# Kernel tuning notes

Measured on AMD Instinct MI355X. Metric: run time of the kernel, lower is better.

Reference implementation:

```python
import jax, jax.numpy as jnp
import numpy as np

B, N, C = 4, 4096, 16
HID, HEADS, OUT = 64, 4, 64
NEG = -1e16

def setup_inputs() -> dict:
    key = jax.random.key(0)
    ks = jax.random.split(key, 7)
    x = jax.random.normal(ks[0], (B, N, C), dtype=jnp.float32)
    # sparse-ish binary adjacency with self-loops, stored dense as in the torch module
    graph = (jax.random.randint(ks[1], (N, N), 0, 2)).astype(jnp.float32)
    graph = jnp.maximum(graph, jnp.eye(N, dtype=jnp.float32))
    # per-head Linear weights (bias=False) and the per-layer bias parameter b
    Ws = jax.random.normal(ks[2], (HEADS, C, HID), dtype=jnp.float32)   # W.weight.T per head
    bs = jax.random.normal(ks[3], (HEADS, HID), dtype=jnp.float32)
    W_out = jax.random.normal(ks[4], (HEADS * HID, OUT), dtype=jnp.float32)
    b_out = jax.random.normal(ks[5], (OUT,), dtype=jnp.float32)
    return {"x": x, "graph": graph, "Ws": Ws, "bs": bs, "W_out": W_out, "b_out": b_out}

def _gat_layer(x, graph, W, b):
    # x: [B,N,Cin], W: [Cin,D], b: [D]
    h = jnp.einsum('bnc,cd->bnd', x, W)                      # [B,N,D]
    s = jnp.einsum('bnd,bmd->bnm', h, h) * graph[None]       # [B,N,N]
    s = jnp.where(s == 0.0, NEG, s)                          # masked_fill(eq 0, -1e16)
    attn = jax.nn.softmax(s, axis=2)
    return jnp.einsum('bnm,bmd->bnd', attn, h) + b

def _leaky_relu(x):
    return jnp.where(x >= 0, x, 0.2 * x)

def reference(x, graph, Ws, bs, W_out, b_out):
    # multi-head layers, concatenated on feature dim (head-major)
    heads = jax.vmap(lambda W, b: _gat_layer(x, graph, W, b))(Ws, bs)  # [H,B,N,D]
    cat = jnp.transpose(heads, (1, 2, 0, 3)).reshape(B, N, HEADS * HID)
    cat = _leaky_relu(cat)
    out = _gat_layer(cat, graph, W_out, b_out)
    return _leaky_relu(out)
```

## Files before the change

### kernel.cpp

```cpp
#include <hip/hip_runtime.h>

typedef unsigned short u16;
typedef unsigned int u32;
typedef unsigned long long u64;
typedef __attribute__((ext_vector_type(8))) short bf16x8;
typedef __attribute__((ext_vector_type(4))) float f32x4;
typedef __attribute__((ext_vector_type(16))) float f32x16;

#define NEGF  -1.0e38f
#define MINIT -1.0e30f
#define LOG2E 1.4426950408889634f

__device__ __forceinline__ u16 f2bf(float x) {
  union { float f; u32 u; } v; v.f = x;
  u32 r = v.u + 0x7fffu + ((v.u >> 16) & 1u);
  return (u16)(r >> 16);
}
__device__ __forceinline__ float bf2f(u16 b) {
  union { u32 u; float f; } v; v.u = ((u32)b) << 16;
  return v.f;
}
__device__ __forceinline__ float bcast(u32 u) {
  union { u32 u; float f; } v; v.u = u; return v.f;
}
__device__ __forceinline__ u32 cvtpk(float a, float b) {
  u32 r;
  asm("v_cvt_pk_bf16_f32 %0, %1, %2" : "=v"(r) : "v"(a), "v"(b));
  return r;
}
__device__ __forceinline__ float vexp2(float x) {
  float r;
  asm("v_exp_f32 %0, %1" : "=v"(r) : "v"(x));
  return r;
}
__device__ __forceinline__ float fmax3(float a, float b, float c) {
  return fmaxf(fmaxf(a, b), c);
}
__device__ __forceinline__ float leaky(float x) { return x >= 0.f ? x : 0.2f * x; }

__device__ __forceinline__ void gload16(const void* g, void* l) {
  __builtin_amdgcn_global_load_lds(
      (const __attribute__((address_space(1))) u32*)(unsigned long long)g,
      (__attribute__((address_space(3))) u32*)(u32)(unsigned long long)l,
      16, 0, 0);
}

#define GRP   1040
#define TILE  8320
#define KA_OFF 0
#define KB_OFF 8320
#define KC_OFF 16640
#define V_OFF  24960
#define SMEM_BYTES 58240

__global__ __launch_bounds__(256) void pack_kernel(const float* __restrict__ graph,
                                                   u64* __restrict__ bits) {
  const int n = blockIdx.x;
  const int w = threadIdx.x >> 6, lane = threadIdx.x & 63;
  const float* gr = graph + (size_t)n * 4096;
  for (int j = 0; j < 16; ++j) {
    const int wd = j * 4 + w;
    u64 m = __ballot(gr[wd * 64 + lane] != 0.0f);
    if (lane == 0) bits[(size_t)wd * 4096 + n] = m;
  }
}

__global__ __launch_bounds__(256) void h1_kernel(const float* __restrict__ x,
                                                 const float* __restrict__ Ws,
                                                 u16* __restrict__ h1a, u16* __restrict__ h1b,
                                                 u16* __restrict__ h1c) {
  const int blk = blockIdx.x;
  const int h = threadIdx.x >> 6, d = threadIdx.x & 63;
  const float* xr = x + (size_t)blk * 16;
  const float* Wp = Ws + h * (16 * 64) + d;
  float acc = 0.f;
  #pragma unroll
  for (int c = 0; c < 16; ++c) acc += xr[c] * Wp[c * 64];
  const int b = blk >> 12, n = blk & 4095;
  const size_t o = ((size_t)(b * 4 + h) * 4096 + n) * 64 + d;
  u16 a = f2bf(acc);
  float r1 = acc - bf2f(a);
  u16 bq = f2bf(r1);
  float r2 = r1 - bf2f(bq);
  h1a[o] = a; h1b[o] = bq; h1c[o] = f2bf(r2);
}

__global__ __launch_bounds__(256) void transpose_kernel(const u16* __restrict__ src,
                                                        u16* __restrict__ dst) {
  const int p = blockIdx.y, n0 = blockIdx.x * 64;
  const u16* s = src + (size_t)p * 4096 * 64;
  u16* d = dst + (size_t)p * 4096 * 64;
  __shared__ u16 tile[64][66];
  const int col = threadIdx.x & 63, r4 = threadIdx.x >> 6;
  #pragma unroll
  for (int i = 0; i < 16; ++i) {
    const int r = i * 4 + r4;
    tile[r][col] = s[(size_t)(n0 + r) * 64 + col];
  }
  __syncthreads();
  const int cs = (col & 51) | ((col & 4) << 1) | ((col & 8) >> 1);
  #pragma unroll
  for (int i = 0; i < 16; ++i) {
    const int r = i * 4 + r4;
    d[(size_t)r * 4096 + n0 + cs] = tile[col][r];
  }
}

__global__ __launch_bounds__(256) void h2_kernel(const float* __restrict__ cat,
                                                 const float* __restrict__ Wout,
                                                 u16* __restrict__ h2a, u16* __restrict__ h2b,
                                                 u16* __restrict__ h2c) {
  const int row = blockIdx.x * 4 + (threadIdx.x >> 6);
  const int d = threadIdx.x & 63;
  const float* cr = cat + (size_t)row * 256;
  float acc = 0.f;
  for (int c4 = 0; c4 < 64; ++c4) {
    const float4 cv = *(const float4*)(cr + c4 * 4);
    acc += cv.x * Wout[(c4 * 4 + 0) * 64 + d];
    acc += cv.y * Wout[(c4 * 4 + 1) * 64 + d];
    acc += cv.z * Wout[(c4 * 4 + 2) * 64 + d];
    acc += cv.w * Wout[(c4 * 4 + 3) * 64 + d];
  }
  const size_t o = (size_t)row * 64 + d;
  u16 a = f2bf(acc);
  float r1 = acc - bf2f(a);
  u16 bq = f2bf(r1);
  float r2 = r1 - bf2f(bq);
  h2a[o] = a; h2b[o] = bq; h2c[o] = f2bf(r2);
}

template <int LAYER>
__global__ __launch_bounds__(256) void attn_kernel(
    const u16* __restrict__ Ha, const u16* __restrict__ Hb, const u16* __restrict__ Hc,
    const u16* __restrict__ HaT, const u16* __restrict__ HbT,
    const u64* __restrict__ bits, const float* __restrict__ bias,
    float* __restrict__ outp, float* __restrict__ pm, float* __restrict__ pl) {
  constexpr int NCH = (LAYER == 1) ? 64 : 16;
  const int orig = blockIdx.x + 32 * blockIdx.y;
  const int sid = (orig & 7) * 64 + (orig >> 3);
  const int bx = sid & 31;
  const int py = sid >> 5;
  const int pass = (LAYER == 1) ? py : (py & 3);
  const int chg0 = (LAYER == 1) ? 0 : ((py >> 2) * 16);

  const int t = threadIdx.x;
  const int wq = t >> 6;
  const int lane = t & 63;
  const int c = lane & 31;
  const int g1 = lane >> 5;
  const int qbase = bx * 128 + wq * 32;
  const int q = qbase + c;
  const size_t poffb = (size_t)pass * (4096 * 64) * 2;

  __shared__ f32x4 smem_v[SMEM_BYTES / 16];
  char* smem = (char*)smem_v;

  const int srow = lane >> 3;
  const int scol = ((lane & 7) ^ srow) << 4;
  const char* gKa = (const char*)Ha + poffb;
  const char* gKb = (const char*)Hb + poffb;
  const char* gKc = (const char*)Hc + poffb;
  const char* gVa = (const char*)HaT + poffb;
  const char* gVb = (const char*)HbT + poffb;

  auto stageK = [&](int chg) {
    const size_t cb = (size_t)chg * 8192;
    #pragma unroll
    for (int ii = 0; ii < 2; ++ii) {
      const int g = wq * 2 + ii;
      const size_t so = cb + (size_t)(g * 8 + srow) * 128 + scol;
      const int dofs = g * GRP;
      gload16(gKa + so, smem + KA_OFF + dofs);
      gload16(gKb + so, smem + KB_OFF + dofs);
      gload16(gKc + so, smem + KC_OFF + dofs);
    }
  };
  auto stageV = [&](int chg, int buf) {
    const char* gsrc = (wq >> 1) ? gVb : gVa;
    char* dbase = smem + V_OFF + buf * 16640 + (wq >> 1) * TILE;
    const size_t cb = (size_t)chg * 128;
    #pragma unroll
    for (int ii = 0; ii < 4; ++ii) {
      const int g = (wq & 1) * 4 + ii;
      const size_t so = cb + (size_t)(g * 8 + srow) * 8192 + scol;
      gload16(gsrc + so, dbase + g * GRP);
    }
  };

  bf16x8 qf[3][4];
  {
    const char* qra = (const char*)Ha + poffb + (size_t)q * 128 + 16 * g1;
    const char* qrb = (const char*)Hb + poffb + (size_t)q * 128 + 16 * g1;
    const char* qrc = (const char*)Hc + poffb + (size_t)q * 128 + 16 * g1;
    #pragma unroll
    for (int kk = 0; kk < 4; ++kk) {
      qf[0][kk] = *(const bf16x8*)(qra + kk * 32);
      qf[1][kk] = *(const bf16x8*)(qrb + kk * 32);
      qf[2][kk] = *(const bf16x8*)(qrc + kk * 32);
    }
  }

  const u64* bqp = bits + q;

  const int swz = (c & 7) << 4;
  int iK[4];
  #pragma unroll
  for (int kk = 0; kk < 4; ++kk)
    iK[kk] = c * 128 + ((c >> 3) << 4) + ((32 * kk + 16 * g1) ^ swz);

  const f32x16 z16 = {};
  f32x16 Of0, Of1;
  #pragma unroll
  for (int r = 0; r < 16; ++r) { Of0[r] = 0.f; Of1[r] = 0.f; }
  float mrow = MINIT, lrow = 0.f;

  stageK(chg0);
  stageV(chg0, 0);
  u64 mcur = bqp[(size_t)chg0 * 4096];
  asm volatile("s_waitcnt vmcnt(0)" ::: "memory");
  __syncthreads();

  #pragma unroll 1
  for (int ch = 0; ch < NCH; ++ch) {
    const int chg = chg0 + ch;
    __builtin_amdgcn_sched_barrier(0);
    f32x16 s0, s1;
    __builtin_amdgcn_s_setprio(1);
    #pragma unroll
    for (int kk = 0; kk < 4; ++kk) {
      const char* kp0 = smem + iK[kk];
      const char* kp1 = smem + 4 * GRP + iK[kk];
      const bf16x8 ka0 = *(const bf16x8*)(kp0 + KA_OFF);
      const bf16x8 kb0 = *(const bf16x8*)(kp0 + KB_OFF);
      const bf16x8 kc0 = *(const bf16x8*)(kp0 + KC_OFF);
      const bf16x8 ka1 = *(const bf16x8*)(kp1 + KA_OFF);
      const bf16x8 kb1 = *(const bf16x8*)(kp1 + KB_OFF);
      const bf16x8 kc1 = *(const bf16x8*)(kp1 + KC_OFF);
      s0 = __builtin_amdgcn_mfma_f32_32x32x16_bf16(ka0, qf[2][kk], kk ? s0 : z16, 0, 0, 0);
      s1 = __builtin_amdgcn_mfma_f32_32x32x16_bf16(ka1, qf[2][kk], kk ? s1 : z16, 0, 0, 0);
      s0 = __builtin_amdgcn_mfma_f32_32x32x16_bf16(kb0, qf[1][kk], s0, 0, 0, 0);
      s1 = __builtin_amdgcn_mfma_f32_32x32x16_bf16(kb1, qf[1][kk], s1, 0, 0, 0);
      s0 = __builtin_amdgcn_mfma_f32_32x32x16_bf16(kc0, qf[0][kk], s0, 0, 0, 0);
      s1 = __builtin_amdgcn_mfma_f32_32x32x16_bf16(kc1, qf[0][kk], s1, 0, 0, 0);
      s0 = __builtin_amdgcn_mfma_f32_32x32x16_bf16(ka0, qf[1][kk], s0, 0, 0, 0);
      s1 = __builtin_amdgcn_mfma_f32_32x32x16_bf16(ka1, qf[1][kk], s1, 0, 0, 0);
      s0 = __builtin_amdgcn_mfma_f32_32x32x16_bf16(kb0, qf[0][kk], s0, 0, 0, 0);
      s1 = __builtin_amdgcn_mfma_f32_32x32x16_bf16(kb1, qf[0][kk], s1, 0, 0, 0);
      s0 = __builtin_amdgcn_mfma_f32_32x32x16_bf16(ka0, qf[0][kk], s0, 0, 0, 0);
      s1 = __builtin_amdgcn_mfma_f32_32x32x16_bf16(ka1, qf[0][kk], s1, 0, 0, 0);
    }
    __builtin_amdgcn_s_setprio(0);
    __builtin_amdgcn_sched_barrier(0);
    __builtin_amdgcn_s_barrier();
    __builtin_amdgcn_sched_barrier(0);
    if (ch + 1 < NCH) {
      stageK(chg + 1);
      stageV(chg + 1, (ch + 1) & 1);
    }
    __builtin_amdgcn_sched_barrier(0);

    const u32 a0 = (u32)(mcur >> (4 * g1));
    const u32 a1 = (u32)(mcur >> (32 + 4 * g1));
    #pragma unroll
    for (int r = 0; r < 16; ++r) {
      const int off = (r & 3) + 8 * (r >> 2);
      s0[r] = ((a0 >> off) & 1u) ? s0[r] : NEGF;
      s1[r] = ((a1 >> off) & 1u) ? s1[r] : NEGF;
    }
    float t0 = fmax3(s0[0], s0[1], s0[2]);
    float t1 = fmax3(s0[3], s0[4], s0[5]);
    float t2 = fmax3(s0[6], s0[7], s0[8]);
    float t3 = fmax3(s0[9], s0[10], s0[11]);
    float t4 = fmax3(s0[12], s0[13], s0[14]);
    float t5 = fmax3(s0[15], s1[0], s1[1]);
    float t6 = fmax3(s1[2], s1[3], s1[4]);
    float t7 = fmax3(s1[5], s1[6], s1[7]);
    float t8 = fmax3(s1[8], s1[9], s1[10]);
    float t9 = fmax3(s1[11], s1[12], s1[13]);
    float ta = fmaxf(s1[14], s1[15]);
    float u0 = fmax3(t0, t1, t2);
    float u1 = fmax3(t3, t4, t5);
    float u2 = fmax3(t6, t7, t8);
    float u3 = fmax3(t9, ta, u0);
    float mm = fmax3(u1, u2, u3);
    mm = fmaxf(mm, __shfl_xor(mm, 32));
    if (!__all(mm <= mrow + 8.f)) {
      const float mn = fmaxf(mrow, mm);
      const float scl = vexp2((mrow - mn) * LOG2E);
      #pragma unroll
      for (int r = 0; r < 16; ++r) { Of0[r] *= scl; Of1[r] *= scl; }
      lrow *= scl;
      mrow = mn;
    }
    if (LAYER == 1) {
      const float mL = mrow * LOG2E;
      #pragma unroll
      for (int r = 0; r < 16; ++r) {
        s0[r] = vexp2(__builtin_fmaf(s0[r], LOG2E, -mL));
        s1[r] = vexp2(__builtin_fmaf(s1[r], LOG2E, -mL));
      }
    } else {
      #pragma unroll
      for (int r = 0; r < 16; ++r) {
        s0[r] = vexp2((s0[r] - mrow) * LOG2E);
        s1[r] = vexp2((s1[r] - mrow) * LOG2E);
      }
    }
    {
      float r4[4];
      #pragma unroll
      for (int j = 0; j < 4; ++j)
        r4[j] = ((s0[4*j] + s0[4*j+1]) + (s0[4*j+2] + s0[4*j+3]))
              + ((s1[4*j] + s1[4*j+1]) + (s1[4*j+2] + s1[4*j+3]));
      float rs = (r4[0] + r4[1]) + (r4[2] + r4[3]);
      rs += __shfl_xor(rs, 32);
      lrow += rs;
    }

    bf16x8 pa[4], pb[4];
    #pragma unroll
    for (int kk = 0; kk < 4; ++kk) {
      const f32x16& sm = (kk >> 1) ? s1 : s0;
      const int rb = 8 * (kk & 1);
      union { u32 w[4]; bf16x8 v; } ua, ub;
      #pragma unroll
      for (int j = 0; j < 4; ++j) {
        const float p0 = sm[rb + 2*j], p1 = sm[rb + 2*j + 1];
        const u32 h = cvtpk(p0, p1);
        ua.w[j] = h;
        const float h0f = bcast(h << 16);
        const float h1f = bcast(h & 0xffff0000u);
        ub.w[j] = cvtpk(p0 - h0f, p1 - h1f);
      }
      pa[kk] = ua.v; pb[kk] = ub.v;
    }

    const char* vbase = smem + V_OFF + (ch & 1) * 16640;
    __builtin_amdgcn_s_setprio(1);
    #pragma unroll
    for (int kk = 0; kk < 4; ++kk) {
      const char* vp0 = vbase + iK[kk];
      const char* vp1 = vbase + 4 * GRP + iK[kk];
      const bf16x8 va0 = *(const bf16x8*)(vp0);
      const bf16x8 vb0 = *(const bf16x8*)(vp0 + TILE);
      const bf16x8 va1 = *(const bf16x8*)(vp1);
      const bf16x8 vb1 = *(const bf16x8*)(vp1 + TILE);
      Of0 = __builtin_amdgcn_mfma_f32_32x32x16_bf16(vb0, pa[kk], Of0, 0, 0, 0);
      Of1 = __builtin_amdgcn_mfma_f32_32x32x16_bf16(vb1, pa[kk], Of1, 0, 0, 0);
      Of0 = __builtin_amdgcn_mfma_f32_32x32x16_bf16(va0, pb[kk], Of0, 0, 0, 0);
      Of1 = __builtin_amdgcn_mfma_f32_32x32x16_bf16(va1, pb[kk], Of1, 0, 0, 0);
      Of0 = __builtin_amdgcn_mfma_f32_32x32x16_bf16(va0, pa[kk], Of0, 0, 0, 0);
      Of1 = __builtin_amdgcn_mfma_f32_32x32x16_bf16(va1, pa[kk], Of1, 0, 0, 0);
    }
    __builtin_amdgcn_s_setprio(0);

    u64 mnxt = 0;
    if (ch + 1 < NCH) mnxt = bqp[(size_t)(chg + 1) * 4096];
    __builtin_amdgcn_sched_barrier(0);
    if (ch + 1 < NCH) {
      asm volatile("s_waitcnt vmcnt(1)" ::: "memory");
    } else {
      asm volatile("s_waitcnt vmcnt(0)" ::: "memory");
    }
    __builtin_amdgcn_sched_barrier(0);
    __builtin_amdgcn_s_barrier();
    mcur = mnxt;
  }

  char* reg = smem + wq * 8704;
  const float inv = (LAYER == 1) ? (1.0f / lrow) : 1.0f;
  #pragma unroll
  for (int dt = 0; dt < 2; ++dt) {
    const f32x16& o = dt ? Of1 : Of0;
    #pragma unroll
    for (int i = 0; i < 4; ++i) {
      f32x4 v;
      v[0] = o[4*i+0] * inv; v[1] = o[4*i+1] * inv;
      v[2] = o[4*i+2] * inv; v[3] = o[4*i+3] * inv;
      *(f32x4*)(reg + c * 272 + (32 * dt + 8 * i + 4 * g1) * 4) = v;
    }
  }
  if (LAYER == 2 && lane < 32) {
    pm[(size_t)py * 4096 + q] = mrow;
    pl[(size_t)py * 4096 + q] = lrow;
  }
  __syncthreads();
  const int d0 = (lane & 15) * 4;
  const float* bp = (LAYER == 1) ? (bias + (pass & 3) * 64) : bias;
  #pragma unroll
  for (int qq = 0; qq < 8; ++qq) {
    const int ql = qq * 4 + (lane >> 4);
    f32x4 v = *(const f32x4*)(reg + ql * 272 + (lane & 15) * 16);
    const int qg = qbase + ql;
    if (LAYER == 1) {
      v[0] = leaky(v[0] + bp[d0 + 0]);
      v[1] = leaky(v[1] + bp[d0 + 1]);
      v[2] = leaky(v[2] + bp[d0 + 2]);
      v[3] = leaky(v[3] + bp[d0 + 3]);
      *(f32x4*)&outp[((size_t)((pass >> 2) * 4096 + qg)) * 256 + (pass & 3) * 64 + d0] = v;
    } else {
      *(f32x4*)&outp[((size_t)py * 4096 + qg) * 64 + d0] = v;
    }
  }
}

__global__ __launch_bounds__(256) void merge_kernel(
    const float* __restrict__ pO, const float* __restrict__ pm, const float* __restrict__ pl,
    const float* __restrict__ bo, float* __restrict__ dout) {
  const int t = threadIdx.x;
  const int d = t & 63;
  const int q = blockIdx.x * 4 + (t >> 6);
  const int pass = blockIdx.y;
  float m[4], l[4], o[4];
  #pragma unroll
  for (int s = 0; s < 4; ++s) {
    const size_t idx = (size_t)(s * 4 + pass) * 4096 + q;
    m[s] = pm[idx]; l[s] = pl[idx];
    o[s] = pO[idx * 64 + d];
  }
  const float M = fmaxf(fmaxf(m[0], m[1]), fmaxf(m[2], m[3]));
  float num = 0.f, den = 0.f;
  #pragma unroll
  for (int s = 0; s < 4; ++s) {
    const float w = exp2f((m[s] - M) * LOG2E);
    num += w * o[s]; den += w * l[s];
  }
  const float r = num / den + bo[d];
  dout[((size_t)pass * 4096 + q) * 64 + d] = leaky(r);
}

extern "C" void kernel_launch(void* const* d_in, const int* in_sizes, int n_in,
                              void* d_out, int out_size, void* d_ws, size_t ws_size,
                              hipStream_t stream) {
  const float* x     = (const float*)d_in[0];
  const float* graph = (const float*)d_in[1];
  const float* Ws    = (const float*)d_in[2];
  const float* bs    = (const float*)d_in[3];
  const float* W_out = (const float*)d_in[4];
  const float* b_out = (const float*)d_in[5];
  char* ws = (char*)d_ws;
  const size_t MiB = 1048576;

  u64* bits   = (u64*)(ws + 0 * MiB);
  u16* h1a    = (u16*)(ws + 2 * MiB);
  u16* h1b    = (u16*)(ws + 10 * MiB);
  u16* h1c    = (u16*)(ws + 18 * MiB);
  u16* h1aT   = (u16*)(ws + 26 * MiB);
  u16* h1bT   = (u16*)(ws + 34 * MiB);
  float* catb = (float*)(ws + 42 * MiB);
  u16* h2a    = (u16*)(ws + 58 * MiB);
  u16* h2b    = (u16*)(ws + 60 * MiB);
  u16* h2c    = (u16*)(ws + 62 * MiB);
  u16* h2aT   = (u16*)(ws + 64 * MiB);
  u16* h2bT   = (u16*)(ws + 66 * MiB);
  float* pO   = (float*)(ws + 2 * MiB);
  float* pmb  = (float*)(ws + 18 * MiB);
  float* plb  = (float*)(ws + 18 * MiB + 262144);

  pack_kernel<<<4096, 256, 0, stream>>>(graph, bits);
  h1_kernel<<<16384, 256, 0, stream>>>(x, Ws, h1a, h1b, h1c);
  transpose_kernel<<<dim3(64, 16), 256, 0, stream>>>(h1a, h1aT);
  transpose_kernel<<<dim3(64, 16), 256, 0, stream>>>(h1b, h1bT);
  attn_kernel<1><<<dim3(32, 16), 256, 0, stream>>>(h1a, h1b, h1c, h1aT, h1bT,
                                                   bits, bs, catb, nullptr, nullptr);
  h2_kernel<<<4096, 256, 0, stream>>>(catb, W_out, h2a, h2b, h2c);
  transpose_kernel<<<dim3(64, 4), 256, 0, stream>>>(h2a, h2aT);
  transpose_kernel<<<dim3(64, 4), 256, 0, stream>>>(h2b, h2bT);
  attn_kernel<2><<<dim3(32, 16), 256, 0, stream>>>(h2a, h2b, h2c, h2aT, h2bT,
                                                   bits, b_out, pO, pmb, plb);
  merge_kernel<<<dim3(1024, 4), 256, 0, stream>>>(pO, pmb, plb, b_out, (float*)d_out);
}
```

Before: 445.0 us.

## Fuse h1 projection with transposes and split softmax into two half-chunks

The h1 projection kernel now processes 64-row tiles per block, stages x in shared memory, keeps weights in registers, and writes the transposed bf16 hi/lo copies directly, replacing two separate transpose launches. In the attention loop, the mask/max/exp/sum/convert and PV MFMA work is split into two halves (s0 then s1), so MFMAs for the first half can overlap the exp work of the second. The split adds an extra max reduction and a possible extra rescale per chunk.

After: 465.5 us. 4.6% more time.

```diff
diff --git a/kernel.cpp b/kernel.cpp
--- a/kernel.cpp
+++ b/kernel.cpp
@@ -68,21 +68,49 @@
 __global__ __launch_bounds__(256) void h1_kernel(const float* __restrict__ x,
                                                  const float* __restrict__ Ws,
                                                  u16* __restrict__ h1a, u16* __restrict__ h1b,
-                                                 u16* __restrict__ h1c) {
-  const int blk = blockIdx.x;
-  const int h = threadIdx.x >> 6, d = threadIdx.x & 63;
-  const float* xr = x + (size_t)blk * 16;
-  const float* Wp = Ws + h * (16 * 64) + d;
-  float acc = 0.f;
-  #pragma unroll
-  for (int c = 0; c < 16; ++c) acc += xr[c] * Wp[c * 64];
-  const int b = blk >> 12, n = blk & 4095;
-  const size_t o = ((size_t)(b * 4 + h) * 4096 + n) * 64 + d;
-  u16 a = f2bf(acc);
-  float r1 = acc - bf2f(a);
-  u16 bq = f2bf(r1);
-  float r2 = r1 - bf2f(bq);
-  h1a[o] = a; h1b[o] = bq; h1c[o] = f2bf(r2);
+                                                 u16* __restrict__ h1c,
+                                                 u16* __restrict__ h1aT, u16* __restrict__ h1bT) {
+  const int n0 = blockIdx.x * 64;
+  const int p  = blockIdx.y;
+  const int b = p >> 2, h = p & 3;
+  const int t = threadIdx.x;
+  const int d = t & 63, rg = t >> 6;
+  __shared__ float xt[64][17];
+  __shared__ u16 ta[64][66];
+  __shared__ u16 tb[64][66];
+  {
+    const float4 v = *(const float4*)(x + ((size_t)b * 4096 + n0 + (t >> 2)) * 16 + (t & 3) * 4);
+    xt[t >> 2][(t & 3) * 4 + 0] = v.x;
+    xt[t >> 2][(t & 3) * 4 + 1] = v.y;
+    xt[t >> 2][(t & 3) * 4 + 2] = v.z;
+    xt[t >> 2][(t & 3) * 4 + 3] = v.w;
+  }
+  float Wd[16];
+  #pragma unroll
+  for (int c = 0; c < 16; ++c) Wd[c] = Ws[h * (16 * 64) + c * 64 + d];
+  __syncthreads();
+  #pragma unroll
+  for (int it = 0; it < 16; ++it) {
+    const int r = it * 4 + rg;
+    float acc = 0.f;
+    #pragma unroll
+    for (int c = 0; c < 16; ++c) acc += xt[r][c] * Wd[c];
+    const size_t o = ((size_t)p * 4096 + n0 + r) * 64 + d;
+    u16 a = f2bf(acc);
+    float r1 = acc - bf2f(a);
+    u16 bq = f2bf(r1);
+    float r2 = r1 - bf2f(bq);
+    h1a[o] = a; h1b[o] = bq; h1c[o] = f2bf(r2);
+    ta[r][d] = a; tb[r][d] = bq;
+  }
+  __syncthreads();
+  const int cs = (d & 51) | ((d & 4) << 1) | ((d & 8) >> 1);
+  #pragma unroll
+  for (int i = 0; i < 16; ++i) {
+    const int dr = i * 4 + rg;
+    h1aT[((size_t)p * 64 + dr) * 4096 + n0 + cs] = ta[d][dr];
+    h1bT[((size_t)p * 64 + dr) * 4096 + n0 + cs] = tb[d][dr];
+  }
 }
 
 __global__ __launch_bounds__(256) void transpose_kernel(const u16* __restrict__ src,
@@ -261,98 +289,81 @@
 
     const u32 a0 = (u32)(mcur >> (4 * g1));
     const u32 a1 = (u32)(mcur >> (32 + 4 * g1));
-    #pragma unroll
-    for (int r = 0; r < 16; ++r) {
-      const int off = (r & 3) + 8 * (r >> 2);
-      s0[r] = ((a0 >> off) & 1u) ? s0[r] : NEGF;
-      s1[r] = ((a1 >> off) & 1u) ? s1[r] : NEGF;
-    }
-    float t0 = fmax3(s0[0], s0[1], s0[2]);
-    float t1 = fmax3(s0[3], s0[4], s0[5]);
-    float t2 = fmax3(s0[6], s0[7], s0[8]);
-    float t3 = fmax3(s0[9], s0[10], s0[11]);
-    float t4 = fmax3(s0[12], s0[13], s0[14]);
-    float t5 = fmax3(s0[15], s1[0], s1[1]);
-    float t6 = fmax3(s1[2], s1[3], s1[4]);
-    float t7 = fmax3(s1[5], s1[6], s1[7]);
-    float t8 = fmax3(s1[8], s1[9], s1[10]);
-    float t9 = fmax3(s1[11], s1[12], s1[13]);
-    float ta = fmaxf(s1[14], s1[15]);
-    float u0 = fmax3(t0, t1, t2);
-    float u1 = fmax3(t3, t4, t5);
-    float u2 = fmax3(t6, t7, t8);
-    float u3 = fmax3(t9, ta, u0);
-    float mm = fmax3(u1, u2, u3);
-    mm = fmaxf(mm, __shfl_xor(mm, 32));
-    if (!__all(mm <= mrow + 8.f)) {
-      const float mn = fmaxf(mrow, mm);
-      const float scl = vexp2((mrow - mn) * LOG2E);
-      #pragma unroll
-      for (int r = 0; r < 16; ++r) { Of0[r] *= scl; Of1[r] *= scl; }
-      lrow *= scl;
-      mrow = mn;
-    }
-    if (LAYER == 1) {
-      const float mL = mrow * LOG2E;
+    const char* vbase = smem + V_OFF + (ch & 1) * 16640;
+    #pragma unroll
+    for (int hs = 0; hs < 2; ++hs) {
+      f32x16& sm = hs ? s1 : s0;
+      const u32 am = hs ? a1 : a0;
       #pragma unroll
       for (int r = 0; r < 16; ++r) {
-        s0[r] = vexp2(__builtin_fmaf(s0[r], LOG2E, -mL));
-        s1[r] = vexp2(__builtin_fmaf(s1[r], LOG2E, -mL));
-      }
-    } else {
+        const int off = (r & 3) + 8 * (r >> 2);
+        sm[r] = ((am >> off) & 1u) ? sm[r] : NEGF;
+      }
+      float t0 = fmax3(sm[0], sm[1], sm[2]);
+      float t1 = fmax3(sm[3], sm[4], sm[5]);
+      float t2 = fmax3(sm[6], sm[7], sm[8]);
+      float t3 = fmax3(sm[9], sm[10], sm[11]);
+      float t4 = fmax3(sm[12], sm[13], sm[14]);
+      float mm = fmax3(fmax3(t0, t1, t2), fmaxf(t3, t4), sm[15]);
+      mm = fmaxf(mm, __shfl_xor(mm, 32));
+      if (!__all(mm <= mrow + 8.f)) {
+        const float mn = fmaxf(mrow, mm);
+        const float scl = vexp2((mrow - mn) * LOG2E);
+        #pragma unroll
+        for (int r = 0; r < 16; ++r) { Of0[r] *= scl; Of1[r] *= scl; }
+        lrow *= scl;
+        mrow = mn;
+      }
+      if (LAYER == 1) {
+        const float mL = mrow * LOG2E;
+        #pragma unroll
+        for (int r = 0; r < 16; ++r) sm[r] = vexp2(__builtin_fmaf(sm[r], LOG2E, -mL));
+      } else {
+        #pragma unroll
+        for (int r = 0; r < 16; ++r) sm[r] = vexp2((sm[r] - mrow) * LOG2E);
+      }
+      {
+        float r4[4];
+        #pragma unroll
+        for (int j = 0; j < 4; ++j)
+          r4[j] = (sm[4*j] + sm[4*j+1]) + (sm[4*j+2] + sm[4*j+3]);
+        float rs = (r4[0] + r4[1]) + (r4[2] + r4[3]);
+        rs += __shfl_xor(rs, 32);
+        lrow += rs;
+      }
+      bf16x8 pa[2], pb[2];
       #pragma unroll
-      for (int r = 0; r < 16; ++r) {
-        s0[r] = vexp2((s0[r] - mrow) * LOG2E);
-        s1[r] = vexp2((s1[r] - mrow) * LOG2E);
-      }
-    }
-    {
-      float r4[4];
+      for (int k2 = 0; k2 < 2; ++k2) {
+        const int rb = 8 * k2;
+        union { u32 w[4]; bf16x8 v; } ua, ub;
+        #pragma unroll
+        for (int j = 0; j < 4; ++j) {
+          const float p0 = sm[rb + 2*j], p1 = sm[rb + 2*j + 1];
+          const u32 hh = cvtpk(p0, p1);
+          ua.w[j] = hh;
+          ub.w[j] = cvtpk(p0 - bcast(hh << 16), p1 - bcast(hh & 0xffff0000u));
+        }
+        pa[k2] = ua.v; pb[k2] = ub.v;
+      }
+      __builtin_amdgcn_s_setprio(1);
       #pragma unroll
-      for (int j = 0; j < 4; ++j)
-        r4[j] = ((s0[4*j] + s0[4*j+1]) + (s0[4*j+2] + s0[4*j+3]))
-              + ((s1[4*j] + s1[4*j+1]) + (s1[4*j+2] + s1[4*j+3]));
-      float rs = (r4[0] + r4[1]) + (r4[2] + r4[3]);
-      rs += __shfl_xor(rs, 32);
-      lrow += rs;
-    }
-
-    bf16x8 pa[4], pb[4];
-    #pragma unroll
-    for (int kk = 0; kk < 4; ++kk) {
-      const f32x16& sm = (kk >> 1) ? s1 : s0;
-      const int rb = 8 * (kk & 1);
-      union { u32 w[4]; bf16x8 v; } ua, ub;
-      #pragma unroll
-      for (int j = 0; j < 4; ++j) {
-        const float p0 = sm[rb + 2*j], p1 = sm[rb + 2*j + 1];
-        const u32 h = cvtpk(p0, p1);
-        ua.w[j] = h;
-        const float h0f = bcast(h << 16);
-        const float h1f = bcast(h & 0xffff0000u);
-        ub.w[j] = cvtpk(p0 - h0f, p1 - h1f);
-      }
-      pa[kk] = ua.v; pb[kk] = ub.v;
-    }
-
-    const char* vbase = smem + V_OFF + (ch & 1) * 16640;
-    __builtin_amdgcn_s_setprio(1);
-    #pragma unroll
-    for (int kk = 0; kk < 4; ++kk) {
-      const char* vp0 = vbase + iK[kk];
-      const char* vp1 = vbase + 4 * GRP + iK[kk];
-      const bf16x8 va0 = *(const bf16x8*)(vp0);
-      const bf16x8 vb0 = *(const bf16x8*)(vp0 + TILE);
-      const bf16x8 va1 = *(const bf16x8*)(vp1);
-      const bf16x8 vb1 = *(const bf16x8*)(vp1 + TILE);
-      Of0 = __builtin_amdgcn_mfma_f32_32x32x16_bf16(vb0, pa[kk], Of0, 0, 0, 0);
-      Of1 = __builtin_amdgcn_mfma_f32_32x32x16_bf16(vb1, pa[kk], Of1, 0, 0, 0);
-      Of0 = __builtin_amdgcn_mfma_f32_32x32x16_bf16(va0, pb[kk], Of0, 0, 0, 0);
-      Of1 = __builtin_amdgcn_mfma_f32_32x32x16_bf16(va1, pb[kk], Of1, 0, 0, 0);
-      Of0 = __builtin_amdgcn_mfma_f32_32x32x16_bf16(va0, pa[kk], Of0, 0, 0, 0);
-      Of1 = __builtin_amdgcn_mfma_f32_32x32x16_bf16(va1, pa[kk], Of1, 0, 0, 0);
-    }
-    __builtin_amdgcn_s_setprio(0);
+      for (int k2 = 0; k2 < 2; ++k2) {
+        const int kk = 2 * hs + k2;
+        const char* vp0 = vbase + iK[kk];
+        const char* vp1 = vbase + 4 * GRP + iK[kk];
+        const bf16x8 va0 = *(const bf16x8*)(vp0);
+        const bf16x8 vb0 = *(const bf16x8*)(vp0 + TILE);
+        const bf16x8 va1 = *(const bf16x8*)(vp1);
+        const bf16x8 vb1 = *(const bf16x8*)(vp1 + TILE);
+        Of0 = __builtin_amdgcn_mfma_f32_32x32x16_bf16(vb0, pa[k2], Of0, 0, 0, 0);
+        Of1 = __builtin_amdgcn_mfma_f32_32x32x16_bf16(vb1, pa[k2], Of1, 0, 0, 0);
+        Of0 = __builtin_amdgcn_mfma_f32_32x32x16_bf16(va0, pb[k2], Of0, 0, 0, 0);
+        Of1 = __builtin_amdgcn_mfma_f32_32x32x16_bf16(va1, pb[k2], Of1, 0, 0, 0);
+        Of0 = __builtin_amdgcn_mfma_f32_32x32x16_bf16(va0, pa[k2], Of0, 0, 0, 0);
+        Of1 = __builtin_amdgcn_mfma_f32_32x32x16_bf16(va1, pa[k2], Of1, 0, 0, 0);
+      }
+      __builtin_amdgcn_s_setprio(0);
+    }
 
     u64 mnxt = 0;
     if (ch + 1 < NCH) mnxt = bqp[(size_t)(chg + 1) * 4096];
@@ -458,9 +469,7 @@
   float* plb  = (float*)(ws + 18 * MiB + 262144);
 
   pack_kernel<<<4096, 256, 0, stream>>>(graph, bits);
-  h1_kernel<<<16384, 256, 0, stream>>>(x, Ws, h1a, h1b, h1c);
-  transpose_kernel<<<dim3(64, 16), 256, 0, stream>>>(h1a, h1aT);
-  transpose_kernel<<<dim3(64, 16), 256, 0, stream>>>(h1b, h1bT);
+  h1_kernel<<<dim3(64, 16), 256, 0, stream>>>(x, Ws, h1a, h1b, h1c, h1aT, h1bT);
   attn_kernel<1><<<dim3(32, 16), 256, 0, stream>>>(h1a, h1b, h1c, h1aT, h1bT,
                                                    bits, bs, catb, nullptr, nullptr);
   h2_kernel<<<4096, 256, 0, stream>>>(catb, W_out, h2a, h2b, h2c);
```
